# Kernel optimization log

Hardware: AMD Instinct MI355X
Metric: run time of the kernel (lower is better)

Reference implementation:

```python
import jax, jax.numpy as jnp
import numpy as np

EPS = 1e-12  # torch.nn.functional.normalize eps


def setup_inputs() -> dict:
    key = jax.random.key(0)
    k1, k2 = jax.random.split(key)
    B, S, H, A = 16, 2048, 1024, 1024
    x = jax.random.normal(k1, (B, S, H), dtype=jnp.float32)
    group_by = jnp.sort(jax.random.randint(k2, (B, S), 0, A), axis=-1)
    return {"x": x, "group_by": group_by, "agg_step": A}


def reference(x, group_by, agg_step):
    # pos_proj[b, a, s] = (group_by[b, s] == a); negative group ids never match.
    pos = jnp.arange(agg_step)[None, :, None] == group_by[:, None, :]  # (B, A, S) bool
    w = pos.astype(x.dtype)
    # L1-normalize over source steps (torch F.normalize p=1 with eps clamp);
    # empty groups -> all-zero row -> zero output, matching original semantics.
    w = w / jnp.maximum(w.sum(axis=-1, keepdims=True), EPS)
    # mean aggregation as batched matmul, same as pos_proj_weight.bmm(x)
    return jnp.einsum('bas,bsh->bah', w, x)  # (B, A, H)
```

## Files before the change

### kernel.cpp

```cpp
#include <hip/hip_runtime.h>


__global__ __launch_bounds__(256) void seq_group_agg_kernel(
    const float* __restrict__ x,
    const int*   __restrict__ gb,
    float*       __restrict__ out,
    int S, int H, int A) {
  const int a = blockIdx.x;
  const int b = blockIdx.y;
  const int* g = gb + (size_t)b * S;

  int lo = 0, hi = S;
  while (lo < hi) { int m = (lo + hi) >> 1; if (g[m] < a) lo = m + 1; else hi = m; }
  const int start = lo;
  hi = S;
  while (lo < hi) { int m = (lo + hi) >> 1; if (g[m] <= a) lo = m + 1; else hi = m; }
  const int end = lo;

  const int cnt = end - start;
  const float scale = (cnt > 0) ? (1.0f / (float)cnt) : 0.0f;

  const int H4 = H >> 2;
  const float4* __restrict__ xb = (const float4*)(x + (size_t)b * S * H);
  float4* __restrict__ ob = (float4*)(out + ((size_t)b * A + a) * H);

  for (int h4 = threadIdx.x; h4 < H4; h4 += blockDim.x) {
    float4 acc = make_float4(0.f, 0.f, 0.f, 0.f);
    for (int s = start; s < end; ++s) {
      const float4 v = xb[(size_t)s * H4 + h4];
      acc.x += v.x; acc.y += v.y; acc.z += v.z; acc.w += v.w;
    }
    acc.x *= scale; acc.y *= scale; acc.z *= scale; acc.w *= scale;
    ob[h4] = acc;
  }
}

extern "C" void kernel_launch(void* const* d_in, const int* in_sizes, int n_in,
                              void* d_out, int out_size, void* d_ws, size_t ws_size,
                              hipStream_t stream) {
  const float* x  = (const float*)d_in[0];
  const int*   gb = (const int*)d_in[1];
  float*       out = (float*)d_out;

  const int BS = in_sizes[1];
  const int H  = in_sizes[0] / BS;
  const int A  = 1024;
  const int B  = (out_size / H) / A;
  const int S  = BS / B;

  dim3 grid(A, B);
  seq_group_agg_kernel<<<grid, 256, 0, stream>>>(x, gb, out, S, H, A);
}
```

Measured before the change: 221.7 us.

## Precompute segment bounds in separate kernel and process 8 groups per block

Moves the per-group binary searches into a dedicated kernel that writes start/end pairs to workspace. The aggregation kernel then handles 8 consecutive groups per block, reading the precomputed bounds, so the redundant per-thread binary search and the per-block launch overhead are removed. The cost is an extra kernel launch, and the block count drops from 16K to 2K, which reduces the parallelism available to hide memory latency. Each thread now works through the 8 segments one after another.

After: 225.4 us. Within noise of the previous version (+1.7%).

```diff
diff --git a/kernel.cpp b/kernel.cpp
--- a/kernel.cpp
+++ b/kernel.cpp
@@ -1,37 +1,53 @@
 #include <hip/hip_runtime.h>
 
 
-__global__ __launch_bounds__(256) void seq_group_agg_kernel(
-    const float* __restrict__ x,
-    const int*   __restrict__ gb,
-    float*       __restrict__ out,
-    int S, int H, int A) {
-  const int a = blockIdx.x;
+constexpr int AG = 8;
+
+__global__ __launch_bounds__(256) void seg_bounds_kernel(
+    const int* __restrict__ gb,
+    int2*      __restrict__ bounds,
+    int S, int A) {
   const int b = blockIdx.y;
-  const int* g = gb + (size_t)b * S;
-
+  const int a = blockIdx.x * blockDim.x + threadIdx.x;
+  if (a >= A) return;
+  const int* __restrict__ g = gb + (size_t)b * S;
   int lo = 0, hi = S;
   while (lo < hi) { int m = (lo + hi) >> 1; if (g[m] < a) lo = m + 1; else hi = m; }
   const int start = lo;
   hi = S;
   while (lo < hi) { int m = (lo + hi) >> 1; if (g[m] <= a) lo = m + 1; else hi = m; }
-  const int end = lo;
+  bounds[(size_t)b * A + a] = make_int2(start, lo);
+}
 
-  const int cnt = end - start;
-  const float scale = (cnt > 0) ? (1.0f / (float)cnt) : 0.0f;
+__global__ __launch_bounds__(256) void seq_group_agg_kernel(
+    const float* __restrict__ x,
+    const int2*  __restrict__ bounds,
+    float*       __restrict__ out,
+    int S, int H4, int A) {
+  const int b  = blockIdx.y;
+  const int a0 = blockIdx.x * AG;
 
-  const int H4 = H >> 2;
-  const float4* __restrict__ xb = (const float4*)(x + (size_t)b * S * H);
-  float4* __restrict__ ob = (float4*)(out + ((size_t)b * A + a) * H);
+  int2 se[AG];
+#pragma unroll
+  for (int j = 0; j < AG; ++j) se[j] = bounds[(size_t)b * A + a0 + j];
+
+  const float4* __restrict__ xb = (const float4*)x + (size_t)b * S * H4;
 
   for (int h4 = threadIdx.x; h4 < H4; h4 += blockDim.x) {
-    float4 acc = make_float4(0.f, 0.f, 0.f, 0.f);
-    for (int s = start; s < end; ++s) {
-      const float4 v = xb[(size_t)s * H4 + h4];
-      acc.x += v.x; acc.y += v.y; acc.z += v.z; acc.w += v.w;
+    float4* __restrict__ ob = (float4*)out + ((size_t)b * A + a0) * H4 + h4;
+#pragma unroll
+    for (int j = 0; j < AG; ++j) {
+      const int start = se[j].x, end = se[j].y;
+      const int cnt = end - start;
+      const float scale = (cnt > 0) ? (1.0f / (float)cnt) : 0.0f;
+      float4 acc = make_float4(0.f, 0.f, 0.f, 0.f);
+      for (int s = start; s < end; ++s) {
+        const float4 v = xb[(size_t)s * H4 + h4];
+        acc.x += v.x; acc.y += v.y; acc.z += v.z; acc.w += v.w;
+      }
+      acc.x *= scale; acc.y *= scale; acc.z *= scale; acc.w *= scale;
+      ob[(size_t)j * H4] = acc;
     }
-    acc.x *= scale; acc.y *= scale; acc.z *= scale; acc.w *= scale;
-    ob[h4] = acc;
   }
 }
 
@@ -48,6 +64,11 @@
   const int B  = (out_size / H) / A;
   const int S  = BS / B;
 
-  dim3 grid(A, B);
-  seq_group_agg_kernel<<<grid, 256, 0, stream>>>(x, gb, out, S, H, A);
+  int2* bounds = (int2*)d_ws;
+
+  dim3 g1((A + 255) / 256, B);
+  seg_bounds_kernel<<<g1, 256, 0, stream>>>(gb, bounds, S, A);
+
+  dim3 g2(A / AG, B);
+  seq_group_agg_kernel<<<g2, 256, 0, stream>>>(x, bounds, out, S, H / 4, A);
 }
```
